# Kernel tuning notes

Measured on AMD Instinct MI355X. Metric: run time of the kernel, lower is better.

## Reference

```python
import jax, jax.numpy as jnp
import numpy as np

B = 256
N_VERTS = 10475
N_JOINTS = 55  # 1 root + 21 body + jaw + 2 eyes + 2*15 hands
NUM_BETAS = 10
NUM_EXPR = 10
POSE_BASIS = (N_JOINTS - 1) * 9  # 486
# SMPL-X kinematic tree (parent index per joint, root = -1)
PARENTS = np.array([-1,0,0,0,1,2,3,4,5,6,7,8,9,9,9,12,13,14,16,17,18,19,15,15,15,
                    20,25,26,20,28,29,20,31,32,20,34,35,20,37,38,
                    21,40,41,21,43,44,21,46,47,21,49,50,21,52,53], dtype=np.int64)


def _rodrigues(aa):
    # axis-angle [..., 3] -> rotation matrix [..., 3, 3]
    angle = jnp.linalg.norm(aa, axis=-1, keepdims=True) + 1e-8
    axis = aa / angle
    x, y, z = axis[..., 0], axis[..., 1], axis[..., 2]
    zero = jnp.zeros_like(x)
    K = jnp.stack([zero, -z, y, z, zero, -x, -y, x, zero], axis=-1).reshape(aa.shape[:-1] + (3, 3))
    s = jnp.sin(angle)[..., None]
    c = jnp.cos(angle)[..., None]
    I = jnp.eye(3, dtype=aa.dtype)
    return I + s * K + (1.0 - c) * (K @ K)


def setup_inputs() -> dict:
    key = jax.random.key(0)
    ks = jax.random.split(key, 16)
    def rots(k, nj, scale=0.2):
        aa = jax.random.normal(k, (B, nj, 3), dtype=jnp.float32) * scale
        return _rodrigues(aa)
    inp = {
        'world_rot': rots(ks[0], 1, 0.5),
        'world_tsl': jax.random.normal(ks[1], (B, 3), dtype=jnp.float32),
        'body_shape': jax.random.normal(ks[2], (B, NUM_BETAS), dtype=jnp.float32),
        'body_pose': rots(ks[3], 21),
        'left_hand_pose': rots(ks[4], 15),
        'right_hand_pose': rots(ks[5], 15),
        'expr_shape': jax.random.normal(ks[6], (B, NUM_EXPR), dtype=jnp.float32),
        'jaw_pose': rots(ks[7], 1),
        'leye_pose': rots(ks[8], 1),
        'reye_pose': rots(ks[9], 1),
        # model buffers (synthetic, SMPL-X-sized)
        'v_template': jax.random.normal(ks[10], (N_VERTS, 3), dtype=jnp.float32) * 0.3,
        'shapedirs': jax.random.normal(ks[11], (N_VERTS, 3, NUM_BETAS), dtype=jnp.float32) * 0.01,
        'expr_dirs': jax.random.normal(ks[12], (N_VERTS, 3, NUM_EXPR), dtype=jnp.float32) * 0.01,
        'posedirs': jax.random.normal(ks[13], (POSE_BASIS, N_VERTS * 3), dtype=jnp.float32) * 0.01,
        'J_regressor': jax.nn.softmax(jax.random.normal(ks[14], (N_JOINTS, N_VERTS), dtype=jnp.float32) * 4.0, axis=-1),
        'lbs_weights': jax.nn.softmax(jax.random.normal(ks[15], (N_VERTS, N_JOINTS), dtype=jnp.float32) * 4.0, axis=-1),
    }
    return inp


def _lbs(world_rot, world_tsl, body_shape, body_pose, left_hand_pose, right_hand_pose,
         expr_shape, jaw_pose, leye_pose, reye_pose,
         v_template, shapedirs, expr_dirs, posedirs, J_regressor, lbs_weights):
    dtype = v_template.dtype
    # full pose: [B, 55, 3, 3]
    full_pose = jnp.concatenate([world_rot, body_pose, jaw_pose, leye_pose, reye_pose,
                                 left_hand_pose, right_hand_pose], axis=1)
    b = full_pose.shape[0]
    # shape + expression blendshapes
    v_shaped = v_template[None] + jnp.einsum('bk,nck->bnc', body_shape, shapedirs) \
               + jnp.einsum('bk,nck->bnc', expr_shape, expr_dirs)
    # rest-pose joints [B, J, 3]
    joints = jnp.einsum('jn,bnc->bjc', J_regressor, v_shaped)
    # pose blendshapes
    ident = jnp.eye(3, dtype=dtype)
    pose_feature = (full_pose[:, 1:] - ident).reshape(b, POSE_BASIS)
    v_posed = v_shaped + (pose_feature @ posedirs).reshape(b, N_VERTS, 3)
    # relative joint locations w.r.t. parent
    rel_joints = joints.at[:, 1:].add(-joints[:, PARENTS[1:]])
    # local 4x4 transforms [B, J, 4, 4]
    top = jnp.concatenate([full_pose, rel_joints[..., None]], axis=-1)  # [B,J,3,4]
    bottom = jnp.broadcast_to(jnp.array([0., 0., 0., 1.], dtype=dtype), (b, N_JOINTS, 1, 4))
    T = jnp.concatenate([top, bottom], axis=2)
    # kinematic chain recurrence (small fixed joint count -> unrolled)
    chain = [T[:, 0]]
    for i in range(1, N_JOINTS):
        chain.append(chain[PARENTS[i]] @ T[:, i])
    A = jnp.stack(chain, axis=1)  # [B, J, 4, 4]
    posed_joints = A[..., :3, 3]
    # remove rest-pose joint offset so A maps rest -> posed
    t_corr = posed_joints - jnp.einsum('bjkl,bjl->bjk', A[..., :3, :3], joints)
    A_rel = A.at[..., :3, 3].set(t_corr)
    # linear blend skinning: per-vertex transform [B, N, 4, 4]
    T_vert = jnp.einsum('nj,bjkl->bnkl', lbs_weights, A_rel)
    verts = jnp.einsum('bnkl,bnl->bnk', T_vert[..., :3, :3], v_posed) + T_vert[..., :3, 3]
    verts = verts + world_tsl[:, None]
    joints_out = posed_joints + world_tsl[:, None]
    return verts, joints_out


def reference(world_rot, world_tsl, body_shape, body_pose, left_hand_pose, right_hand_pose,
              expr_shape, jaw_pose, leye_pose, reye_pose,
              v_template, shapedirs, expr_dirs, posedirs, J_regressor, lbs_weights):
    return _lbs(world_rot, world_tsl, body_shape, body_pose, left_hand_pose, right_hand_pose,
                expr_shape, jaw_pose, leye_pose, reye_pose,
                v_template, shapedirs, expr_dirs, posedirs, J_regressor, lbs_weights)
```

## Files before the change

### kernel.cpp

```cpp
#include <hip/hip_runtime.h>
#include <stdint.h>

#define BATCH 256
#define NV 10475
#define NVP 10496
#define NJ 55
#define PB 486
#define KS 506
#define VC (NV*3)
#define KP 512
#define BKC 32
#define NCHUNK 16
#define BN 64
#define JCH 8
#define JCHUNK 1312

typedef short bf16x8 __attribute__((ext_vector_type(8)));
typedef float f32x4  __attribute__((ext_vector_type(4)));

__constant__ int c_parents[NJ] = {
  -1,0,0,0,1,2,3,4,5,6,7,8,9,9,9,12,13,14,16,17,18,19,15,15,15,
  20,25,26,20,28,29,20,31,32,20,34,35,20,37,38,21,40,41,21,43,44,
  21,46,47,21,49,50,21,52,53};

__constant__ int c_depth[NJ] = {
  0,1,1,1,2,2,2,3,3,3,4,4,4,4,4,5,5,5,6,6,7,7,6,6,6,
  8,9,10,8,9,10,8,9,10,8,9,10,8,9,10,
  8,9,10,8,9,10,8,9,10,8,9,10,8,9,10};

__device__ __forceinline__ unsigned short f2bf(float x){
  uint32_t u = __float_as_uint(x);
  uint32_t r = (u + 0x7fffu + ((u >> 16) & 1u)) >> 16;
  return (unsigned short)r;
}
__device__ __forceinline__ float bf2f(unsigned short h){
  return __uint_as_float(((uint32_t)h) << 16);
}

__global__ __launch_bounds__(256) void k_prep(
    const float* __restrict__ lw, const float* __restrict__ sd,
    const float* __restrict__ ed, unsigned short* __restrict__ lwb,
    float* __restrict__ sdedT) {
  int bid = blockIdx.x;
  const int LWB_BLOCKS = (NVP*64)/256;
  if (bid < LWB_BLOCKS) {
    int idx = bid*256 + threadIdx.x;
    int n = idx >> 6, j = idx & 63;
    float v = (n < NV && j < NJ) ? lw[(size_t)n*NJ + j] : 0.f;
    unsigned short hi = f2bf(v);
    float lo = v - bf2f(hi);
    lwb[idx] = hi;
    lwb[(size_t)NVP*64 + idx] = f2bf(lo);
  } else {
    int idx = (bid - LWB_BLOCKS)*256 + threadIdx.x;
    if (idx >= 20*VC) return;
    int r = idx / VC, col = idx - r*VC;
    int n = col/3, c = col - n*3;
    float v = (r < 10) ? sd[(size_t)n*30 + c*10 + r]
                       : ed[(size_t)n*30 + c*10 + (r-10)];
    sdedT[idx] = v;
  }
}

__device__ __forceinline__ const float* pose_src(int j, int b,
    const float* wrot, const float* bpose, const float* jaw, const float* leye,
    const float* reye, const float* lhand, const float* rhand) {
  if (j==0)  return wrot  + b*9;
  if (j<=21) return bpose + (b*21 + (j-1))*9;
  if (j==22) return jaw   + b*9;
  if (j==23) return leye  + b*9;
  if (j==24) return reye  + b*9;
  if (j<=39) return lhand + (b*15 + (j-25))*9;
  return rhand + (b*15 + (j-40))*9;
}

__global__ __launch_bounds__(512) void k_posefeat(
    const float* __restrict__ bpose, const float* __restrict__ jaw,
    const float* __restrict__ leye, const float* __restrict__ reye,
    const float* __restrict__ lhand, const float* __restrict__ rhand,
    const float* __restrict__ bs, const float* __restrict__ es,
    unsigned short* __restrict__ pfb) {
  int b = blockIdx.x, t = threadIdx.x;
  unsigned short o = 0;
  if (t < PB){
    int jj = t/9, rc = t - jj*9;
    const float* rs = pose_src(jj+1, b, nullptr, bpose, jaw, leye, reye, lhand, rhand);
    float v = rs[rc];
    if (rc==0 || rc==4 || rc==8) v -= 1.0f;
    o = f2bf(v);
  } else if (t < 496){
    o = f2bf(bs[b*10 + (t-486)]);
  } else if (t < KS){
    o = f2bf(es[b*10 + (t-496)]);
  }
  pfb[(size_t)b*KP + t] = o;
}

__global__ __launch_bounds__(256) void k_jsmall(
    const float* __restrict__ jreg, const float* __restrict__ sd,
    const float* __restrict__ ed, const float* __restrict__ vt,
    float* __restrict__ part) {
  int ch = blockIdx.x, j = blockIdx.y;
  int t = threadIdx.x;
  float acc[63];
  #pragma unroll
  for (int s=0;s<63;s++) acc[s]=0.f;
  int n0 = ch*JCHUNK, nend = min(n0+JCHUNK, NV);
  for (int n = n0 + t; n < nend; n += 256){
    float w = jreg[(size_t)j*NV + n];
    const float* sp = sd + (size_t)n*30;
    const float* ep = ed + (size_t)n*30;
    const float* vp = vt + (size_t)n*3;
    #pragma unroll
    for (int c=0;c<3;c++){
      #pragma unroll
      for (int q=0;q<10;q++){
        acc[c*21+q]    += w*sp[c*10+q];
        acc[c*21+10+q] += w*ep[c*10+q];
      }
      acc[c*21+20] += w*vp[c];
    }
  }
  #pragma unroll
  for (int s=0;s<63;s++){
    float a = acc[s];
    #pragma unroll
    for (int d=32; d>=1; d>>=1) a += __shfl_xor(a,d);
    acc[s]=a;
  }
  __shared__ float red[4][63];
  int w = t>>6, l = t&63;
  if (l==0){
    #pragma unroll
    for (int s=0;s<63;s++) red[w][s]=acc[s];
  }
  __syncthreads();
  if (t < 63){
    float a = red[0][t]+red[1][t]+red[2][t]+red[3][t];
    part[((size_t)j*JCH+ch)*63 + t] = a;
  }
}

__global__ __launch_bounds__(192) void k_joints2(
    const float* __restrict__ part, const float* __restrict__ bs,
    const float* __restrict__ es, float* __restrict__ joints) {
  int b = blockIdx.x, t = threadIdx.x;
  if (t >= NJ*3) return;
  int j = t/3, c = t - j*3;
  float S[21];
  #pragma unroll
  for (int q=0;q<21;q++) S[q]=0.f;
  for (int ch=0; ch<JCH; ch++){
    const float* p = part + ((size_t)j*JCH+ch)*63 + c*21;
    #pragma unroll
    for (int q=0;q<21;q++) S[q] += p[q];
  }
  float a = S[20];
  #pragma unroll
  for (int q=0;q<10;q++) a += S[q]*bs[b*10+q] + S[10+q]*es[b*10+q];
  joints[(size_t)b*NJ*3 + t] = a;
}

__global__ __launch_bounds__(256) void k_chain(
    const float* __restrict__ wrot, const float* __restrict__ bpose,
    const float* __restrict__ jaw, const float* __restrict__ leye,
    const float* __restrict__ reye, const float* __restrict__ lhand,
    const float* __restrict__ rhand, const float* __restrict__ wtsl,
    const float* __restrict__ joints,
    unsigned short* __restrict__ arelb, float* __restrict__ jout) {
  const int w = threadIdx.x >> 6, lane = threadIdx.x & 63;
  const int b = blockIdx.x*4 + w;
  const int j = lane;
  const bool act = (j < NJ);

  float R[9] = {1.f,0.f,0.f, 0.f,1.f,0.f, 0.f,0.f,1.f};
  if (act){
    const float* rs = pose_src(j, b, wrot, bpose, jaw, leye, reye, lhand, rhand);
    #pragma unroll
    for (int i=0;i<9;i++) R[i]=rs[i];
  }
  float jx=0.f, jy=0.f, jz=0.f;
  if (act){
    const float* jb = joints + (size_t)b*NJ*3 + j*3;
    jx=jb[0]; jy=jb[1]; jz=jb[2];
  }
  int par = act ? c_parents[j] : 0;
  if (par < 0) par = 0;
  float px = __shfl(jx, par), py = __shfl(jy, par), pz = __shfl(jz, par);
  float t0, t1, t2;
  if (j == 0){ t0=jx; t1=jy; t2=jz; }
  else       { t0=jx-px; t1=jy-py; t2=jz-pz; }

  float M[12];
  #pragma unroll
  for (int r=0;r<3;r++){
    M[r*4+0]=R[r*3+0]; M[r*4+1]=R[r*3+1]; M[r*4+2]=R[r*3+2]; M[r*4+3]= (r==0?t0:(r==1?t1:t2));
  }
  int dep = act ? c_depth[j] : 99;

  #pragma unroll
  for (int L=1; L<=10; L++){
    float pm[12];
    #pragma unroll
    for (int i=0;i<12;i++) pm[i] = __shfl(M[i], par);
    if (dep == L){
      #pragma unroll
      for (int r=0;r<3;r++){
        float p0=pm[r*4+0], p1=pm[r*4+1], p2=pm[r*4+2], p3=pm[r*4+3];
        M[r*4+0] = p0*R[0]+p1*R[3]+p2*R[6];
        M[r*4+1] = p0*R[1]+p1*R[4]+p2*R[7];
        M[r*4+2] = p0*R[2]+p1*R[5]+p2*R[8];
        M[r*4+3] = p0*t0 + p1*t1 + p2*t2 + p3;
      }
    }
  }

  float wx=wtsl[b*3+0], wy=wtsl[b*3+1], wz=wtsl[b*3+2];
  if (act){
    jout[((size_t)b*NJ+j)*3+0] = M[3]  + wx;
    jout[((size_t)b*NJ+j)*3+1] = M[7]  + wy;
    jout[((size_t)b*NJ+j)*3+2] = M[11] + wz;
  }
  float A[12];
  #pragma unroll
  for (int r=0;r<3;r++){
    A[r*4+0]=M[r*4+0]; A[r*4+1]=M[r*4+1]; A[r*4+2]=M[r*4+2];
    A[r*4+3]=M[r*4+3] - (M[r*4+0]*jx + M[r*4+1]*jy + M[r*4+2]*jz);
  }
  unsigned short* ah = arelb + (size_t)(b*2+0)*16*64;
  unsigned short* al = arelb + (size_t)(b*2+1)*16*64;
  #pragma unroll
  for (int e=0;e<16;e++){
    float v = (e < 12 && act) ? A[e] : 0.f;
    unsigned short hi = f2bf(v);
    float lo = v - bf2f(hi);
    ah[e*64 + j] = hi;
    al[e*64 + j] = f2bf(lo);
  }
}

__global__ __launch_bounds__(256, 2) void k_vposed(
    const float* __restrict__ pd, const float* __restrict__ sdedT,
    const float* __restrict__ vt, const unsigned short* __restrict__ pfb,
    float* __restrict__ vsh) {
  const int tid  = threadIdx.x;
  const int w    = tid >> 6, lane = tid & 63;
  const int m16  = lane & 15, quad = lane >> 4;
  const int col0 = blockIdx.x * BN;

  f32x4 acc[4][4];
  #pragma unroll
  for (int i=0;i<4;i++)
    #pragma unroll
    for (int j=0;j<4;j++) acc[i][j] = (f32x4){0.f,0.f,0.f,0.f};

  int bcol[4];
  #pragma unroll
  for (int ni=0;ni<4;ni++) bcol[ni] = min(col0 + ni*16 + m16, VC-1);

  const unsigned short* pfa = pfb + (size_t)(w*64 + m16)*KP + quad*8;

  #pragma unroll 2
  for (int c=0; c<15; c++){
    const int k0 = c*BKC;
    bf16x8 a[4];
    #pragma unroll
    for (int mi=0;mi<4;mi++)
      a[mi] = *((const bf16x8*)(pfa + (size_t)mi*16*KP + k0));
    union { bf16x8 v; unsigned short s[8]; } bb[4];
    #pragma unroll
    for (int ni=0;ni<4;ni++){
      #pragma unroll
      for (int j=0;j<8;j++){
        int kk = k0 + quad*8 + j;
        bb[ni].s[j] = f2bf(pd[(size_t)kk*VC + bcol[ni]]);
      }
    }
    #pragma unroll
    for (int mi=0;mi<4;mi++)
      #pragma unroll
      for (int ni=0;ni<4;ni++)
        acc[mi][ni] = __builtin_amdgcn_mfma_f32_16x16x32_bf16(
                          a[mi], bb[ni].v, acc[mi][ni], 0, 0, 0);
  }
  {
    const int k0 = 15*BKC;
    bf16x8 a[4];
    #pragma unroll
    for (int mi=0;mi<4;mi++)
      a[mi] = *((const bf16x8*)(pfa + (size_t)mi*16*KP + k0));
    union { bf16x8 v; unsigned short s[8]; } bb[4];
    #pragma unroll
    for (int ni=0;ni<4;ni++){
      #pragma unroll
      for (int j=0;j<8;j++){
        int kk = k0 + quad*8 + j;
        float f = 0.f;
        if (kk < PB)      f = pd[(size_t)kk*VC + bcol[ni]];
        else if (kk < KS) f = sdedT[(size_t)(kk-PB)*VC + bcol[ni]];
        bb[ni].s[j] = f2bf(f);
      }
    }
    #pragma unroll
    for (int mi=0;mi<4;mi++)
      #pragma unroll
      for (int ni=0;ni<4;ni++)
        acc[mi][ni] = __builtin_amdgcn_mfma_f32_16x16x32_bf16(
                          a[mi], bb[ni].v, acc[mi][ni], 0, 0, 0);
  }
  #pragma unroll
  for (int mi=0;mi<4;mi++){
    int rbase = w*64 + mi*16 + quad*4;
    #pragma unroll
    for (int ni=0;ni<4;ni++){
      int col = col0 + ni*16 + m16;
      if (col < VC){
        float vtc = vt[col];
        #pragma unroll
        for (int r=0;r<4;r++)
          vsh[(size_t)(rbase + r)*VC + col] = acc[mi][ni][r] + vtc;
      }
    }
  }
}

__global__ __launch_bounds__(256) void k_verts(
    const unsigned short* __restrict__ lwb, const unsigned short* __restrict__ arelb,
    const float* __restrict__ wtsl, float* __restrict__ out) {
  const int tid = threadIdx.x, w = tid >> 6, lane = tid & 63;
  const int m16 = lane & 15, quad = lane >> 4;
  const int n0 = blockIdx.x*64;
  const int b0 = blockIdx.y*16;

  bf16x8 lwh[4][2], lwl[4][2];
  #pragma unroll
  for (int vt4=0; vt4<4; vt4++){
    int row = n0 + vt4*16 + m16;
    #pragma unroll
    for (int kc=0;kc<2;kc++){
      lwh[vt4][kc] = *((const bf16x8*)(lwb + (size_t)row*64 + kc*32 + quad*8));
      lwl[vt4][kc] = *((const bf16x8*)(lwb + (size_t)NVP*64 + (size_t)row*64 + kc*32 + quad*8));
    }
  }
  for (int bi=0; bi<4; bi++){
    const int b = b0 + w*4 + bi;
    bf16x8 ah[2], al[2];
    #pragma unroll
    for (int kc=0;kc<2;kc++){
      ah[kc] = *((const bf16x8*)(arelb + ((size_t)(b*2+0)*16 + m16)*64 + kc*32 + quad*8));
      al[kc] = *((const bf16x8*)(arelb + ((size_t)(b*2+1)*16 + m16)*64 + kc*32 + quad*8));
    }
    float vx[4], vy[4], vz[4];
    #pragma unroll
    for (int vt4=0; vt4<4; vt4++){
      int n = n0 + vt4*16 + m16;
      const float* vp = out + ((size_t)b*NV + n)*3;
      bool ok = (n < NV);
      vx[vt4] = ok ? vp[0] : 0.f;
      vy[vt4] = ok ? vp[1] : 0.f;
      vz[vt4] = ok ? vp[2] : 0.f;
    }
    f32x4 acc[4];
    #pragma unroll
    for (int vt4=0; vt4<4; vt4++) acc[vt4] = (f32x4){0.f,0.f,0.f,0.f};
    #pragma unroll
    for (int vt4=0; vt4<4; vt4++){
      #pragma unroll
      for (int kc=0;kc<2;kc++){
        acc[vt4] = __builtin_amdgcn_mfma_f32_16x16x32_bf16(ah[kc], lwh[vt4][kc], acc[vt4], 0,0,0);
        acc[vt4] = __builtin_amdgcn_mfma_f32_16x16x32_bf16(al[kc], lwh[vt4][kc], acc[vt4], 0,0,0);
        acc[vt4] = __builtin_amdgcn_mfma_f32_16x16x32_bf16(ah[kc], lwl[vt4][kc], acc[vt4], 0,0,0);
      }
    }
    float wk = (quad < 3) ? wtsl[b*3 + quad] : 0.f;
    #pragma unroll
    for (int vt4=0; vt4<4; vt4++){
      int n = n0 + vt4*16 + m16;
      float p = acc[vt4][0]*vx[vt4] + acc[vt4][1]*vy[vt4]
              + acc[vt4][2]*vz[vt4] + acc[vt4][3] + wk;
      if (quad < 3 && n < NV)
        out[((size_t)b*NV + n)*3 + quad] = p;
    }
  }
}

extern "C" void kernel_launch(void* const* d_in, const int* in_sizes, int n_in,
                              void* d_out, int out_size, void* d_ws, size_t ws_size,
                              hipStream_t stream) {
  const float* wrot   = (const float*)d_in[0];
  const float* wtsl   = (const float*)d_in[1];
  const float* bshape = (const float*)d_in[2];
  const float* bpose  = (const float*)d_in[3];
  const float* lhand  = (const float*)d_in[4];
  const float* rhand  = (const float*)d_in[5];
  const float* eshape = (const float*)d_in[6];
  const float* jaw    = (const float*)d_in[7];
  const float* leye   = (const float*)d_in[8];
  const float* reye   = (const float*)d_in[9];
  const float* vt     = (const float*)d_in[10];
  const float* sd     = (const float*)d_in[11];
  const float* ed     = (const float*)d_in[12];
  const float* pd     = (const float*)d_in[13];
  const float* jreg   = (const float*)d_in[14];
  const float* lw     = (const float*)d_in[15];
  float* out = (float*)d_out;

  float* vsh  = out;
  float* jout = out + (size_t)BATCH*NV*3;

  float* ws     = (float*)d_ws;
  float* joints = ws;
  float* part   = joints + (size_t)BATCH*NJ*3;
  float* sdedT  = part   + (size_t)NJ*JCH*63;
  unsigned short* pfb   = (unsigned short*)(sdedT + (size_t)20*VC);
  unsigned short* lwb   = pfb + (size_t)BATCH*KP;
  unsigned short* arelb = lwb + (size_t)2*NVP*64;

  const int PREP_BLOCKS = (NVP*64)/256 + (20*VC + 255)/256;

  k_prep    <<<PREP_BLOCKS, 256, 0, stream>>>(lw, sd, ed, lwb, sdedT);
  k_posefeat<<<BATCH, 512, 0, stream>>>(bpose, jaw, leye, reye, lhand, rhand,
                                        bshape, eshape, pfb);
  k_jsmall  <<<dim3(JCH, NJ), 256, 0, stream>>>(jreg, sd, ed, vt, part);
  k_joints2 <<<BATCH, 192, 0, stream>>>(part, bshape, eshape, joints);
  k_chain   <<<64, 256, 0, stream>>>(wrot, bpose, jaw, leye, reye, lhand, rhand,
                                     wtsl, joints, arelb, jout);
  k_vposed  <<<(VC+BN-1)/BN, 256, 0, stream>>>(pd, sdedT, vt, pfb, vsh);
  k_verts   <<<dim3(NVP/64, 16), 256, 0, stream>>>(lwb, arelb, wtsl, out);
}
```

Measured before the change: 270.6 us.

## Drop shapedir transpose pass and transpose skinning transforms through LDS

The prep kernel no longer transposes shapedirs/expr_dirs into a workspace buffer. The last K chunk of the vposed GEMM now reads those coefficients directly from the original layout. In k_verts, the MFMA accumulators holding per-vertex 3x4 transforms are staged through shared memory so each lane owns one vertex. Each lane then reads its vertex once and writes all three output coordinates, instead of every lane re-reading xyz for four vertices and writing one strided component. This trims the prep traffic and the redundant global loads in the skinning pass, at the cost of LDS traffic and strided reads in the tail K chunk.

```diff
diff --git a/kernel.cpp b/kernel.cpp
--- a/kernel.cpp
+++ b/kernel.cpp
@@ -38,28 +38,14 @@
 }
 
 __global__ __launch_bounds__(256) void k_prep(
-    const float* __restrict__ lw, const float* __restrict__ sd,
-    const float* __restrict__ ed, unsigned short* __restrict__ lwb,
-    float* __restrict__ sdedT) {
-  int bid = blockIdx.x;
-  const int LWB_BLOCKS = (NVP*64)/256;
-  if (bid < LWB_BLOCKS) {
-    int idx = bid*256 + threadIdx.x;
-    int n = idx >> 6, j = idx & 63;
-    float v = (n < NV && j < NJ) ? lw[(size_t)n*NJ + j] : 0.f;
-    unsigned short hi = f2bf(v);
-    float lo = v - bf2f(hi);
-    lwb[idx] = hi;
-    lwb[(size_t)NVP*64 + idx] = f2bf(lo);
-  } else {
-    int idx = (bid - LWB_BLOCKS)*256 + threadIdx.x;
-    if (idx >= 20*VC) return;
-    int r = idx / VC, col = idx - r*VC;
-    int n = col/3, c = col - n*3;
-    float v = (r < 10) ? sd[(size_t)n*30 + c*10 + r]
-                       : ed[(size_t)n*30 + c*10 + (r-10)];
-    sdedT[idx] = v;
-  }
+    const float* __restrict__ lw, unsigned short* __restrict__ lwb) {
+  int idx = blockIdx.x*256 + threadIdx.x;
+  int n = idx >> 6, j = idx & 63;
+  float v = (n < NV && j < NJ) ? lw[(size_t)n*NJ + j] : 0.f;
+  unsigned short hi = f2bf(v);
+  float lo = v - bf2f(hi);
+  lwb[idx] = hi;
+  lwb[(size_t)NVP*64 + idx] = f2bf(lo);
 }
 
 __device__ __forceinline__ const float* pose_src(int j, int b,
@@ -240,9 +226,9 @@
 }
 
 __global__ __launch_bounds__(256, 2) void k_vposed(
-    const float* __restrict__ pd, const float* __restrict__ sdedT,
-    const float* __restrict__ vt, const unsigned short* __restrict__ pfb,
-    float* __restrict__ vsh) {
+    const float* __restrict__ pd, const float* __restrict__ sd,
+    const float* __restrict__ ed, const float* __restrict__ vt,
+    const unsigned short* __restrict__ pfb, float* __restrict__ vsh) {
   const int tid  = threadIdx.x;
   const int w    = tid >> 6, lane = tid & 63;
   const int m16  = lane & 15, quad = lane >> 4;
@@ -292,12 +278,18 @@
     union { bf16x8 v; unsigned short s[8]; } bb[4];
     #pragma unroll
     for (int ni=0;ni<4;ni++){
+      int n3 = bcol[ni]/3, c3 = bcol[ni] - n3*3;
+      const float* sp = sd + (size_t)n3*30 + c3*10;
+      const float* ep = ed + (size_t)n3*30 + c3*10;
       #pragma unroll
       for (int j=0;j<8;j++){
         int kk = k0 + quad*8 + j;
         float f = 0.f;
         if (kk < PB)      f = pd[(size_t)kk*VC + bcol[ni]];
-        else if (kk < KS) f = sdedT[(size_t)(kk-PB)*VC + bcol[ni]];
+        else if (kk < KS){
+          int q = kk - PB;
+          f = (q < 10) ? sp[q] : ep[q-10];
+        }
         bb[ni].s[j] = f2bf(f);
       }
     }
@@ -327,10 +319,12 @@
 __global__ __launch_bounds__(256) void k_verts(
     const unsigned short* __restrict__ lwb, const unsigned short* __restrict__ arelb,
     const float* __restrict__ wtsl, float* __restrict__ out) {
+  __shared__ float sT[4*64*17];
   const int tid = threadIdx.x, w = tid >> 6, lane = tid & 63;
   const int m16 = lane & 15, quad = lane >> 4;
   const int n0 = blockIdx.x*64;
   const int b0 = blockIdx.y*16;
+  float* myT = &sT[w*64*17];
 
   bf16x8 lwh[4][2], lwl[4][2];
   #pragma unroll
@@ -342,6 +336,9 @@
       lwl[vt4][kc] = *((const bf16x8*)(lwb + (size_t)NVP*64 + (size_t)row*64 + kc*32 + quad*8));
     }
   }
+  const int nA = n0 + lane;
+  const bool okA = (nA < NV);
+
   for (int bi=0; bi<4; bi++){
     const int b = b0 + w*4 + bi;
     bf16x8 ah[2], al[2];
@@ -350,16 +347,11 @@
       ah[kc] = *((const bf16x8*)(arelb + ((size_t)(b*2+0)*16 + m16)*64 + kc*32 + quad*8));
       al[kc] = *((const bf16x8*)(arelb + ((size_t)(b*2+1)*16 + m16)*64 + kc*32 + quad*8));
     }
-    float vx[4], vy[4], vz[4];
-    #pragma unroll
-    for (int vt4=0; vt4<4; vt4++){
-      int n = n0 + vt4*16 + m16;
-      const float* vp = out + ((size_t)b*NV + n)*3;
-      bool ok = (n < NV);
-      vx[vt4] = ok ? vp[0] : 0.f;
-      vy[vt4] = ok ? vp[1] : 0.f;
-      vz[vt4] = ok ? vp[2] : 0.f;
-    }
+    const float* vp = out + ((size_t)b*NV + nA)*3;
+    float vx = okA ? vp[0] : 0.f;
+    float vy = okA ? vp[1] : 0.f;
+    float vz = okA ? vp[2] : 0.f;
+
     f32x4 acc[4];
     #pragma unroll
     for (int vt4=0; vt4<4; vt4++) acc[vt4] = (f32x4){0.f,0.f,0.f,0.f};
@@ -372,14 +364,22 @@
         acc[vt4] = __builtin_amdgcn_mfma_f32_16x16x32_bf16(ah[kc], lwl[vt4][kc], acc[vt4], 0,0,0);
       }
     }
-    float wk = (quad < 3) ? wtsl[b*3 + quad] : 0.f;
     #pragma unroll
     for (int vt4=0; vt4<4; vt4++){
-      int n = n0 + vt4*16 + m16;
-      float p = acc[vt4][0]*vx[vt4] + acc[vt4][1]*vy[vt4]
-              + acc[vt4][2]*vz[vt4] + acc[vt4][3] + wk;
-      if (quad < 3 && n < NV)
-        out[((size_t)b*NV + n)*3 + quad] = p;
+      #pragma unroll
+      for (int r=0;r<4;r++)
+        myT[(vt4*16 + m16)*17 + quad*4 + r] = acc[vt4][r];
+    }
+    float T[12];
+    const float* Tp = &myT[lane*17];
+    #pragma unroll
+    for (int e=0;e<12;e++) T[e] = Tp[e];
+    if (okA){
+      float tx=wtsl[b*3+0], ty=wtsl[b*3+1], tz=wtsl[b*3+2];
+      float* op = out + ((size_t)b*NV + nA)*3;
+      op[0] = T[0]*vx + T[1]*vy + T[2] *vz + T[3]  + tx;
+      op[1] = T[4]*vx + T[5]*vy + T[6] *vz + T[7]  + ty;
+      op[2] = T[8]*vx + T[9]*vy + T[10]*vz + T[11] + tz;
     }
   }
 }
@@ -411,20 +411,19 @@
   float* ws     = (float*)d_ws;
   float* joints = ws;
   float* part   = joints + (size_t)BATCH*NJ*3;
-  float* sdedT  = part   + (size_t)NJ*JCH*63;
-  unsigned short* pfb   = (unsigned short*)(sdedT + (size_t)20*VC);
+  unsigned short* pfb   = (unsigned short*)(part + (size_t)NJ*JCH*63);
   unsigned short* lwb   = pfb + (size_t)BATCH*KP;
   unsigned short* arelb = lwb + (size_t)2*NVP*64;
 
-  const int PREP_BLOCKS = (NVP*64)/256 + (20*VC + 255)/256;
-
-  k_prep    <<<PREP_BLOCKS, 256, 0, stream>>>(lw, sd, ed, lwb, sdedT);
+  const int PREP_BLOCKS = (NVP*64)/256;
+
+  k_prep    <<<PREP_BLOCKS, 256, 0, stream>>>(lw, lwb);
   k_posefeat<<<BATCH, 512, 0, stream>>>(bpose, jaw, leye, reye, lhand, rhand,
                                         bshape, eshape, pfb);
   k_jsmall  <<<dim3(JCH, NJ), 256, 0, stream>>>(jreg, sd, ed, vt, part);
   k_joints2 <<<BATCH, 192, 0, stream>>>(part, bshape, eshape, joints);
   k_chain   <<<64, 256, 0, stream>>>(wrot, bpose, jaw, leye, reye, lhand, rhand,
                                      wtsl, joints, arelb, jout);
-  k_vposed  <<<(VC+BN-1)/BN, 256, 0, stream>>>(pd, sdedT, vt, pfb, vsh);
+  k_vposed  <<<(VC+BN-1)/BN, 256, 0, stream>>>(pd, sd, ed, vt, pfb, vsh);
   k_verts   <<<dim3(NVP/64, 16), 256, 0, stream>>>(lwb, arelb, wtsl, out);
 }
```

New measurement: 246.9 us. 1.1x faster.
